# Kernel tuning notes

Measured on AMD Instinct MI355X. Metric: run time of the kernel, lower is better.

## Reference

```python
import jax, jax.numpy as jnp
import numpy as np
import math

B, T, E = 2, 2048, 1024
H = 16
D = E // H  # head_dim = 64

def setup_inputs() -> dict:
    key = jax.random.key(0)
    k1, k2, k3, k4, k5 = jax.random.split(key, 5)
    s = 0.02
    return {
        "x": jax.random.normal(k1, (B, T, E), dtype=jnp.float32),
        "W_attn": jax.random.normal(k2, (E, 3 * E), dtype=jnp.float32) * s,
        "b_attn": jax.random.normal(k3, (3 * E,), dtype=jnp.float32) * s,
        "W_proj": jax.random.normal(k4, (E, E), dtype=jnp.float32) * s,
        "b_proj": jax.random.normal(k5, (E,), dtype=jnp.float32) * s,
    }

def reference(x, W_attn, b_attn, W_proj, b_proj):
    Bx, Tx, Ex = x.shape
    qkv = x @ W_attn + b_attn                      # [B,T,3E]
    q, k, v = jnp.split(qkv, 3, axis=2)
    # [B,T,E] -> [B,H,T,D]
    def heads(t):
        return t.reshape(Bx, Tx, H, D).transpose(0, 2, 1, 3)
    q, k, v = heads(q), heads(k), heads(v)
    scores = jnp.einsum('bhqd,bhkd->bhqk', q, k) / math.sqrt(D)
    causal = jnp.tril(jnp.ones((Tx, Tx), dtype=bool))
    scores = jnp.where(causal, scores, -jnp.inf)
    attn = jax.nn.softmax(scores, axis=-1)
    out = jnp.einsum('bhqk,bhkd->bhqd', attn, v)   # [B,H,T,D]
    out = out.transpose(0, 2, 1, 3).reshape(Bx, Tx, Ex)
    return out @ W_proj + b_proj
```

## Files before the change

### kernel.cpp

```cpp
#include <hip/hip_runtime.h>


typedef unsigned short u16;
typedef __bf16 bf8 __attribute__((ext_vector_type(8)));
typedef float f32x4 __attribute__((ext_vector_type(4)));

struct __align__(8) u16x4s { u16 v[4]; };

__device__ __forceinline__ u16 f2b(float f) {
    union { float f; unsigned u; } x{f};
    unsigned r = x.u + 0x7fffu + ((x.u >> 16) & 1u);
    return (u16)(r >> 16);
}

__device__ __forceinline__ f32x4 mfma16(bf8 a, bf8 b, f32x4 c) {
    return __builtin_amdgcn_mfma_f32_16x16x32_bf16(a, b, c, 0, 0, 0);
}

__device__ __forceinline__ float fexp2(float x) {
    return __builtin_amdgcn_exp2f(x);
}

__device__ __forceinline__ void gload_lds16(const u16* g, u16* l) {
    __builtin_amdgcn_global_load_lds(
        (__attribute__((address_space(1))) void*)(g),
        (__attribute__((address_space(3))) void*)(l), 16, 0, 0);
}

__global__ __launch_bounds__(256) void k_cvt(const float* __restrict__ in,
                                             u16* __restrict__ out, int n4) {
    int i = blockIdx.x * 256 + threadIdx.x;
    if (i >= n4) return;
    float4 v = ((const float4*)in)[i];
    ushort4 o;
    o.x = f2b(v.x); o.y = f2b(v.y); o.z = f2b(v.z); o.w = f2b(v.w);
    ((ushort4*)out)[i] = o;
}

__global__ __launch_bounds__(256) void k_tr(const float* __restrict__ in,
                                            u16* __restrict__ out, int K, int N) {
    __shared__ float tile[64][65];
    int k0 = blockIdx.x * 64, n0 = blockIdx.y * 64;
    int t = threadIdx.x, c = t & 63, r0 = t >> 6;
#pragma unroll
    for (int i = 0; i < 16; ++i) {
        int r = r0 + i * 4;
        tile[r][c] = in[(size_t)(k0 + r) * N + n0 + c];
    }
    __syncthreads();
#pragma unroll
    for (int i = 0; i < 16; ++i) {
        int r = r0 + i * 4;
        out[(size_t)(n0 + r) * K + k0 + c] = f2b(tile[c][r]);
    }
}

#define GEMM_CORE(Aptr, Bptr)                                                  \
    int tid = threadIdx.x;                                                     \
    int w = tid >> 6, lane = tid & 63, l16 = lane & 15, quad = lane >> 4;      \
    int m0 = blockIdx.x * 128, n0 = blockIdx.y * 128;                          \
    int wr = (w >> 1) * 64, wc = (w & 1) * 64;                                 \
    __shared__ u16 As[128 * 32];                                               \
    __shared__ u16 Bs[128 * 32];                                               \
    f32x4 acc[4][4];                                                           \
    _Pragma("unroll") for (int mi = 0; mi < 4; ++mi)                           \
        _Pragma("unroll") for (int ni = 0; ni < 4; ++ni)                       \
            _Pragma("unroll") for (int r = 0; r < 4; ++r) acc[mi][ni][r] = 0.f;\
    int srow = tid >> 2;                                                       \
    int scol = (tid & 3) * 8;                                                  \
    const u16* gA = Aptr + (size_t)(m0 + srow) * 1024 + scol;                  \
    const u16* gB = Bptr + (size_t)(n0 + srow) * 1024 + scol;                  \
    u16* lA0 = As + tid * 8;  u16* lA1 = As + (256 + tid) * 8;                 \
    u16* lB0 = Bs + tid * 8;  u16* lB1 = Bs + (256 + tid) * 8;                 \
    for (int k0 = 0; k0 < 1024; k0 += 32) {                                    \
        gload_lds16(gA, lA0);                                                  \
        gload_lds16(gA + 64 * 1024, lA1);                                      \
        gload_lds16(gB, lB0);                                                  \
        gload_lds16(gB + 64 * 1024, lB1);                                      \
        gA += 32; gB += 32;                                                    \
        __syncthreads();                                                       \
        bf8 af[4], bf[4];                                                      \
        _Pragma("unroll") for (int mi = 0; mi < 4; ++mi)                       \
            af[mi] = *(const bf8*)(As + (wr + mi * 16 + l16) * 32 + quad * 8); \
        _Pragma("unroll") for (int ni = 0; ni < 4; ++ni)                       \
            bf[ni] = *(const bf8*)(Bs + (wc + ni * 16 + l16) * 32 + quad * 8); \
        _Pragma("unroll") for (int mi = 0; mi < 4; ++mi)                       \
            _Pragma("unroll") for (int ni = 0; ni < 4; ++ni)                   \
                acc[mi][ni] = mfma16(af[mi], bf[ni], acc[mi][ni]);             \
        __syncthreads();                                                       \
    }

__global__ __launch_bounds__(256) void k_qkv(const u16* __restrict__ Xb,
                                             const u16* __restrict__ WtA,
                                             const float* __restrict__ ba,
                                             u16* __restrict__ Qb,
                                             u16* __restrict__ Kb,
                                             u16* __restrict__ Vtb) {
    GEMM_CORE(Xb, WtA)
    int sel = n0 >> 10;
    u16* dst = sel == 0 ? Qb : (sel == 1 ? Kb : Vtb);
    const float qs = 0.18033688011112042f;
#pragma unroll
    for (int ni = 0; ni < 4; ++ni) {
        int n = n0 + wc + ni * 16 + l16;
        float bias = ba[n];
        int h = (n & 1023) >> 6;
        int d = n & 63;
#pragma unroll
        for (int mi = 0; mi < 4; ++mi)
#pragma unroll
            for (int r = 0; r < 4; ++r) {
                int m = m0 + wr + mi * 16 + quad * 4 + r;
                int bb = m >> 11, tt = m & 2047;
                float v = acc[mi][ni][r] + bias;
                size_t hb = (size_t)(bb * 16 + h);
                if (sel == 2)
                    dst[hb * 131072 + (size_t)(tt >> 6) * 4096 + d * 64 + (tt & 63)] = f2b(v);
                else
                    dst[(hb * 2048 + tt) * 64 + d] =
                        f2b(sel == 0 ? v * qs : v);
            }
    }
}

__global__ __launch_bounds__(256) void k_proj(const u16* __restrict__ AO,
                                              const u16* __restrict__ WtP,
                                              const float* __restrict__ bp,
                                              float* __restrict__ out) {
    GEMM_CORE(AO, WtP)
#pragma unroll
    for (int ni = 0; ni < 4; ++ni) {
        int n = n0 + wc + ni * 16 + l16;
        float bias = bp[n];
#pragma unroll
        for (int mi = 0; mi < 4; ++mi)
#pragma unroll
            for (int r = 0; r < 4; ++r) {
                int m = m0 + wr + mi * 16 + quad * 4 + r;
                out[(size_t)m * 1024 + n] = acc[mi][ni][r] + bias;
            }
    }
}


#define STAGE(KT, B) do {                                                     \
    int ci0_ = tid, ci1_ = 256 + tid;                                         \
    const u16* kt_ = Kh + (size_t)(KT) * 4096;                                \
    gload_lds16(kt_ + (ci0_ >> 3) * 64 +                                      \
                (((ci0_ & 7) ^ ((ci0_ >> 5) & 7)) * 8), Ks[B] + ci0_ * 8);    \
    gload_lds16(kt_ + (ci1_ >> 3) * 64 +                                      \
                (((ci1_ & 7) ^ ((ci1_ >> 5) & 7)) * 8), Ks[B] + ci1_ * 8);    \
    const u16* vt_ = Vh + (size_t)(KT) * 4096;                                \
    gload_lds16(vt_ + (ci0_ >> 3) * 64 +                                      \
                (((ci0_ & 7) ^ ((ci0_ >> 3) & 7)) * 8), Vs[B] + ci0_ * 8);    \
    gload_lds16(vt_ + (ci1_ >> 3) * 64 +                                      \
                (((ci1_ & 7) ^ ((ci1_ >> 3) & 7)) * 8), Vs[B] + ci1_ * 8);    \
} while (0)

#define QK_SOFT(KT, KF, QF0, QF1, LI, QROW, KTM, PBUF) do {                   \
    int kb_ = (KT) * 64;                                                      \
    bool diag_ = ((KT) == (KTM));                                             \
    f32x4 s_acc[4];                                                           \
    _Pragma("unroll") for (int s = 0; s < 4; ++s)                             \
        _Pragma("unroll") for (int r = 0; r < 4; ++r) s_acc[s][r] = 0.f;      \
    _Pragma("unroll") for (int sub = 0; sub < 4; ++sub) {                     \
        s_acc[sub] = mfma16(QF0, KF[sub][0], s_acc[sub]);                     \
        s_acc[sub] = mfma16(QF1, KF[sub][1], s_acc[sub]);                     \
    }                                                                         \
    _Pragma("unroll") for (int r = 0; r < 4; ++r) {                           \
        float p[4];                                                           \
        if (diag_) {                                                          \
            int qg_ = (QROW) + quad * 4 + r;                                  \
            _Pragma("unroll") for (int sub = 0; sub < 4; ++sub) {             \
                int key_ = kb_ + 4 * l16 + sub;                               \
                p[sub] = fexp2(key_ <= qg_ ? s_acc[sub][r] : -1e30f);         \
            }                                                                 \
        } else {                                                              \
            _Pragma("unroll") for (int sub = 0; sub < 4; ++sub)               \
                p[sub] = fexp2(s_acc[sub][r]);                                \
        }                                                                     \
        LI[r] += (p[0] + p[1]) + (p[2] + p[3]);                               \
        u16x4s pk_;                                                           \
        _Pragma("unroll") for (int sub = 0; sub < 4; ++sub)                   \
            pk_.v[sub] = f2b(p[sub]);                                         \
        *(u16x4s*)&PBUF[quad * 4 + r][l16 * 4] = pk_;       \
    }                                                                         \
} while (0)

#define PV_ACC(VF, PBUF, OACC) do {                                           \
    bf8 pf0 = *(const bf8*)&PBUF[l16][quad * 8];                              \
    bf8 pf1 = *(const bf8*)&PBUF[l16][32 + quad * 8];                         \
    _Pragma("unroll") for (int dt = 0; dt < 4; ++dt) {                        \
        OACC[dt] = mfma16(pf0, VF[dt][0], OACC[dt]);                          \
        OACC[dt] = mfma16(pf1, VF[dt][1], OACC[dt]);                          \
    }                                                                         \
} while (0)

__global__ __launch_bounds__(256, 2) void k_attn(const u16* __restrict__ Qb,
                                                 const u16* __restrict__ Kb,
                                                 const u16* __restrict__ Vtb,
                                                 u16* __restrict__ AO) {
    int id = blockIdx.x;
    int bh = (id & 7) * 4 + ((id >> 3) & 3);
    int t  = 15 - (id >> 5);
    int tid = threadIdx.x;
    int w = tid >> 6, lane = tid & 63, l16 = lane & 15, quad = lane >> 4;

    const u16* Qh = Qb  + (size_t)bh * 2048 * 64;
    const u16* Kh = Kb  + (size_t)bh * 2048 * 64;
    const u16* Vh = Vtb + (size_t)bh * 131072;

    int qrA = t * 64 + w * 16;
    int qrB = qrA + 1024;
    int ktmaxA = t, ktmaxB = t + 16;

    __shared__ u16 Ks[2][64 * 64];
    __shared__ u16 Vs[2][64 * 64];
    __shared__ u16 P[4][2][16][72];

    bf8 qfA0 = *(const bf8*)(Qh + (size_t)(qrA + l16) * 64 + quad * 8);
    bf8 qfA1 = *(const bf8*)(Qh + (size_t)(qrA + l16) * 64 + 32 + quad * 8);
    bf8 qfB0 = *(const bf8*)(Qh + (size_t)(qrB + l16) * 64 + quad * 8);
    bf8 qfB1 = *(const bf8*)(Qh + (size_t)(qrB + l16) * 64 + 32 + quad * 8);

    float l_iA[4] = {0.f, 0.f, 0.f, 0.f};
    float l_iB[4] = {0.f, 0.f, 0.f, 0.f};
    f32x4 o_accA[4], o_accB[4];
#pragma unroll
    for (int dt = 0; dt < 4; ++dt)
#pragma unroll
        for (int r = 0; r < 4; ++r) { o_accA[dt][r] = 0.f; o_accB[dt][r] = 0.f; }

    int xsw = (l16 & 7) * 8;

    STAGE(0, 0);
    for (int kt = 0; kt <= ktmaxB; ++kt) {
        int pb = kt & 1;
        __syncthreads();

        bf8 kf[4][2], vf[4][2];
        const u16* kb_ = Ks[pb];
        const u16* vb_ = Vs[pb];
#pragma unroll
        for (int sub = 0; sub < 4; ++sub)
#pragma unroll
            for (int ks = 0; ks < 2; ++ks)
                kf[sub][ks] = *(const bf8*)(kb_ + (4 * l16 + sub) * 64 +
                                            (((ks * 32 + quad * 8)) ^ xsw));
#pragma unroll
        for (int dt = 0; dt < 4; ++dt)
#pragma unroll
            for (int ks = 0; ks < 2; ++ks)
                vf[dt][ks] = *(const bf8*)(vb_ + (dt * 16 + l16) * 64 +
                                           (((ks * 32 + quad * 8)) ^ xsw));

        if (kt < ktmaxB) STAGE(kt + 1, pb ^ 1);

        bool aAct = (kt <= ktmaxA);
        if (aAct) QK_SOFT(kt, kf, qfA0, qfA1, l_iA, qrA, ktmaxA, P[w][0]);
        QK_SOFT(kt, kf, qfB0, qfB1, l_iB, qrB, ktmaxB, P[w][1]);
        asm volatile("s_waitcnt lgkmcnt(0)" ::: "memory");
        if (aAct) PV_ACC(vf, P[w][0], o_accA);
        PV_ACC(vf, P[w][1], o_accB);
    }

    float linvA[4], linvB[4];
#pragma unroll
    for (int r = 0; r < 4; ++r) {
        float la = l_iA[r], lb = l_iB[r];
        la += __shfl_xor(la, 1, 64); lb += __shfl_xor(lb, 1, 64);
        la += __shfl_xor(la, 2, 64); lb += __shfl_xor(lb, 2, 64);
        la += __shfl_xor(la, 4, 64); lb += __shfl_xor(lb, 4, 64);
        la += __shfl_xor(la, 8, 64); lb += __shfl_xor(lb, 8, 64);
        linvA[r] = __builtin_amdgcn_rcpf(la);
        linvB[r] = __builtin_amdgcn_rcpf(lb);
    }

    int b = bh >> 4, h = bh & 15;
#pragma unroll
    for (int dt = 0; dt < 4; ++dt)
#pragma unroll
        for (int r = 0; r < 4; ++r) {
            int off = quad * 4 + r;
            size_t rowA = (size_t)b * 2048 + qrA + off;
            size_t rowB = (size_t)b * 2048 + qrB + off;
            AO[rowA * 1024 + h * 64 + dt * 16 + l16] = f2b(o_accA[dt][r] * linvA[r]);
            AO[rowB * 1024 + h * 64 + dt * 16 + l16] = f2b(o_accB[dt][r] * linvB[r]);
        }
}

extern "C" void kernel_launch(void* const* d_in, const int* in_sizes, int n_in,
                              void* d_out, int out_size, void* d_ws, size_t ws_size,
                              hipStream_t stream) {
    const float* x  = (const float*)d_in[0];
    const float* Wa = (const float*)d_in[1];
    const float* ba = (const float*)d_in[2];
    const float* Wp = (const float*)d_in[3];
    const float* bp = (const float*)d_in[4];
    float* out = (float*)d_out;

    char* ws = (char*)d_ws;
    const size_t MB = 1024 * 1024;
    u16* Xb  = (u16*)(ws);
    u16* WtA = (u16*)(ws + 8  * MB);
    u16* WtP = (u16*)(ws + 14 * MB);
    u16* Qb  = (u16*)(ws + 16 * MB);
    u16* Kb  = (u16*)(ws + 24 * MB);
    u16* Vtb = (u16*)(ws + 32 * MB);
    u16* AO  = Xb;

    k_cvt <<<dim3(4096),    dim3(256), 0, stream>>>(x, Xb, 1048576);
    k_tr  <<<dim3(16, 48),  dim3(256), 0, stream>>>(Wa, WtA, 1024, 3072);
    k_tr  <<<dim3(16, 16),  dim3(256), 0, stream>>>(Wp, WtP, 1024, 1024);
    k_qkv <<<dim3(32, 24),  dim3(256), 0, stream>>>(Xb, WtA, ba, Qb, Kb, Vtb);
    k_attn<<<dim3(512),     dim3(256), 0, stream>>>(Qb, Kb, Vtb, AO);
    k_proj<<<dim3(32, 8),   dim3(256), 0, stream>>>(AO, WtP, bp, out);
}
```

Measured before the change: 202.6 us.

## Double-buffer GEMM LDS tiles with XOR swizzle and merge prep kernels

The three conversion and transpose kernels are merged into one launch, removing two kernel launches and their gaps. The shared GEMM core now double-buffers its LDS tiles and issues the next stage's global-to-LDS loads before the MFMAs, so memory latency overlaps with compute and only one barrier is needed per iteration. An XOR swizzle on the LDS column is meant to reduce bank conflicts on fragment reads, and launch bounds request 3 blocks per CU. In exchange LDS use doubles, and relying on a single barrier makes correctness depend on how the async loads are ordered against it.

```diff
diff --git a/kernel.cpp b/kernel.cpp
--- a/kernel.cpp
+++ b/kernel.cpp
@@ -27,21 +27,27 @@
         (__attribute__((address_space(3))) void*)(l), 16, 0, 0);
 }
 
-__global__ __launch_bounds__(256) void k_cvt(const float* __restrict__ in,
-                                             u16* __restrict__ out, int n4) {
-    int i = blockIdx.x * 256 + threadIdx.x;
-    if (i >= n4) return;
-    float4 v = ((const float4*)in)[i];
-    ushort4 o;
-    o.x = f2b(v.x); o.y = f2b(v.y); o.z = f2b(v.z); o.w = f2b(v.w);
-    ((ushort4*)out)[i] = o;
-}
-
-__global__ __launch_bounds__(256) void k_tr(const float* __restrict__ in,
-                                            u16* __restrict__ out, int K, int N) {
+__global__ __launch_bounds__(256) void k_prep(const float* __restrict__ x,
+                                              const float* __restrict__ Wa,
+                                              const float* __restrict__ Wp,
+                                              u16* __restrict__ Xb,
+                                              u16* __restrict__ WtA,
+                                              u16* __restrict__ WtP) {
     __shared__ float tile[64][65];
-    int k0 = blockIdx.x * 64, n0 = blockIdx.y * 64;
-    int t = threadIdx.x, c = t & 63, r0 = t >> 6;
+    int id = blockIdx.x, t = threadIdx.x;
+    if (id < 4096) {
+        int i = id * 256 + t;
+        float4 v = ((const float4*)x)[i];
+        ushort4 o;
+        o.x = f2b(v.x); o.y = f2b(v.y); o.z = f2b(v.z); o.w = f2b(v.w);
+        ((ushort4*)Xb)[i] = o;
+        return;
+    }
+    const float* in; u16* out; int N, j;
+    if (id < 4864) { j = id - 4096; in = Wa; out = WtA; N = 3072; }
+    else           { j = id - 4864; in = Wp; out = WtP; N = 1024; }
+    int k0 = (j & 15) * 64, n0 = (j >> 4) * 64;
+    int c = t & 63, r0 = t >> 6;
 #pragma unroll
     for (int i = 0; i < 16; ++i) {
         int r = r0 + i * 4;
@@ -51,51 +57,57 @@
 #pragma unroll
     for (int i = 0; i < 16; ++i) {
         int r = r0 + i * 4;
-        out[(size_t)(n0 + r) * K + k0 + c] = f2b(tile[c][r]);
-    }
-}
+        out[(size_t)(n0 + r) * 1024 + k0 + c] = f2b(tile[c][r]);
+    }
+}
+
+#define GEMM_STAGE(GA0, GA1, GB0, GB1, K, B)                                   \
+    do {                                                                       \
+        gload_lds16(GA0 + (K), As[B] + tid * 8);                               \
+        gload_lds16(GA1 + (K), As[B] + (256 + tid) * 8);                       \
+        gload_lds16(GB0 + (K), Bs[B] + tid * 8);                               \
+        gload_lds16(GB1 + (K), Bs[B] + (256 + tid) * 8);                       \
+    } while (0)
 
 #define GEMM_CORE(Aptr, Bptr)                                                  \
     int tid = threadIdx.x;                                                     \
     int w = tid >> 6, lane = tid & 63, l16 = lane & 15, quad = lane >> 4;      \
     int m0 = blockIdx.x * 128, n0 = blockIdx.y * 128;                          \
     int wr = (w >> 1) * 64, wc = (w & 1) * 64;                                 \
-    __shared__ u16 As[128 * 32];                                               \
-    __shared__ u16 Bs[128 * 32];                                               \
+    __shared__ u16 As[2][128 * 32];                                            \
+    __shared__ u16 Bs[2][128 * 32];                                            \
     f32x4 acc[4][4];                                                           \
     _Pragma("unroll") for (int mi = 0; mi < 4; ++mi)                           \
         _Pragma("unroll") for (int ni = 0; ni < 4; ++ni)                       \
             _Pragma("unroll") for (int r = 0; r < 4; ++r) acc[mi][ni][r] = 0.f;\
-    int srow = tid >> 2;                                                       \
-    int scol = (tid & 3) * 8;                                                  \
-    const u16* gA = Aptr + (size_t)(m0 + srow) * 1024 + scol;                  \
-    const u16* gB = Bptr + (size_t)(n0 + srow) * 1024 + scol;                  \
-    u16* lA0 = As + tid * 8;  u16* lA1 = As + (256 + tid) * 8;                 \
-    u16* lB0 = Bs + tid * 8;  u16* lB1 = Bs + (256 + tid) * 8;                 \
-    for (int k0 = 0; k0 < 1024; k0 += 32) {                                    \
-        gload_lds16(gA, lA0);                                                  \
-        gload_lds16(gA + 64 * 1024, lA1);                                      \
-        gload_lds16(gB, lB0);                                                  \
-        gload_lds16(gB + 64 * 1024, lB1);                                      \
-        gA += 32; gB += 32;                                                    \
-        __syncthreads();                                                       \
+    int srow0 = tid >> 2, srow1 = 64 + srow0;                                  \
+    int slc = ((tid & 3) ^ ((tid >> 3) & 3)) * 8;      \
+    const u16* gA0 = Aptr + (size_t)(m0 + srow0) * 1024 + slc;                 \
+    const u16* gA1 = Aptr + (size_t)(m0 + srow1) * 1024 + slc;                 \
+    const u16* gB0 = Bptr + (size_t)(n0 + srow0) * 1024 + slc;                 \
+    const u16* gB1 = Bptr + (size_t)(n0 + srow1) * 1024 + slc;                 \
+    int cq = (quad ^ ((l16 >> 1) & 3)) * 8;               \
+    GEMM_STAGE(gA0, gA1, gB0, gB1, 0, 0);                                      \
+    for (int it = 0; it < 32; ++it) {                                          \
+        int pb = it & 1;                                                       \
+        __syncthreads();                           \
         bf8 af[4], bf[4];                                                      \
         _Pragma("unroll") for (int mi = 0; mi < 4; ++mi)                       \
-            af[mi] = *(const bf8*)(As + (wr + mi * 16 + l16) * 32 + quad * 8); \
+            af[mi] = *(const bf8*)(As[pb] + (wr + mi * 16 + l16) * 32 + cq);   \
         _Pragma("unroll") for (int ni = 0; ni < 4; ++ni)                       \
-            bf[ni] = *(const bf8*)(Bs + (wc + ni * 16 + l16) * 32 + quad * 8); \
+            bf[ni] = *(const bf8*)(Bs[pb] + (wc + ni * 16 + l16) * 32 + cq);   \
+        if (it < 31) GEMM_STAGE(gA0, gA1, gB0, gB1, (it + 1) * 32, pb ^ 1);    \
         _Pragma("unroll") for (int mi = 0; mi < 4; ++mi)                       \
             _Pragma("unroll") for (int ni = 0; ni < 4; ++ni)                   \
                 acc[mi][ni] = mfma16(af[mi], bf[ni], acc[mi][ni]);             \
-        __syncthreads();                                                       \
-    }
-
-__global__ __launch_bounds__(256) void k_qkv(const u16* __restrict__ Xb,
-                                             const u16* __restrict__ WtA,
-                                             const float* __restrict__ ba,
-                                             u16* __restrict__ Qb,
-                                             u16* __restrict__ Kb,
-                                             u16* __restrict__ Vtb) {
+    }
+
+__global__ __launch_bounds__(256, 3) void k_qkv(const u16* __restrict__ Xb,
+                                                const u16* __restrict__ WtA,
+                                                const float* __restrict__ ba,
+                                                u16* __restrict__ Qb,
+                                                u16* __restrict__ Kb,
+                                                u16* __restrict__ Vtb) {
     GEMM_CORE(Xb, WtA)
     int sel = n0 >> 10;
     u16* dst = sel == 0 ? Qb : (sel == 1 ? Kb : Vtb);
@@ -123,10 +135,10 @@
     }
 }
 
-__global__ __launch_bounds__(256) void k_proj(const u16* __restrict__ AO,
-                                              const u16* __restrict__ WtP,
-                                              const float* __restrict__ bp,
-                                              float* __restrict__ out) {
+__global__ __launch_bounds__(256, 3) void k_proj(const u16* __restrict__ AO,
+                                                 const u16* __restrict__ WtP,
+                                                 const float* __restrict__ bp,
+                                                 float* __restrict__ out) {
     GEMM_CORE(AO, WtP)
 #pragma unroll
     for (int ni = 0; ni < 4; ++ni) {
@@ -309,9 +321,7 @@
     u16* Vtb = (u16*)(ws + 32 * MB);
     u16* AO  = Xb;
 
-    k_cvt <<<dim3(4096),    dim3(256), 0, stream>>>(x, Xb, 1048576);
-    k_tr  <<<dim3(16, 48),  dim3(256), 0, stream>>>(Wa, WtA, 1024, 3072);
-    k_tr  <<<dim3(16, 16),  dim3(256), 0, stream>>>(Wp, WtP, 1024, 1024);
+    k_prep<<<dim3(5120),    dim3(256), 0, stream>>>(x, Wa, Wp, Xb, WtA, WtP);
     k_qkv <<<dim3(32, 24),  dim3(256), 0, stream>>>(Xb, WtA, ba, Qb, Kb, Vtb);
     k_attn<<<dim3(512),     dim3(256), 0, stream>>>(Qb, Kb, Vtb, AO);
     k_proj<<<dim3(32, 8),   dim3(256), 0, stream>>>(AO, WtP, bp, out);
```

Measured after the change: 175.3 us. 1.16x faster.
